# Optimization experiments

Measured on AMD Instinct MI355X. Metric: run time of the kernel, lower is better.

## Reference

```python
import jax, jax.numpy as jnp
import numpy as np

B, T, C, P = 512, 365, 10, 64  # batch, num_steps, input_dim, num_prototypes


def setup_inputs() -> dict:
    key = jax.random.key(0)
    k1, k2, k3, k4 = jax.random.split(key, 4)
    input_seq = jax.random.normal(k1, (B, T, C), dtype=jnp.float32)
    # binary observation mask (some dates missing)
    mask = (jax.random.uniform(k2, (B, T)) > 0.1).astype(jnp.float32)
    label = jax.random.randint(k3, (B,), 0, P)
    prototypes = jax.random.normal(k4, (P, T, C), dtype=jnp.float32)
    return {"input_seq": input_seq, "mask": mask, "label": label,
            "prototypes": prototypes}


def reference(input_seq, mask, label, prototypes):
    # distances[b,p] = sum_{t,c} mask[b,t] * (x[b,t,c] - proto[p,t,c])^2
    # expanded so we never materialize the [B,P,T,C] broadcast:
    #   = sum mask*x^2  - 2*sum mask*x*p + sum mask*p^2
    x2 = jnp.einsum('btc,btc,bt->b', input_seq, input_seq, mask)          # [B]
    xp = jnp.einsum('btc,bt,ptc->bp', input_seq, mask, prototypes)        # [B,P]
    p2 = jnp.einsum('bt,ptc,ptc->bp', mask, prototypes, prototypes)       # [B,P]
    distances = x2[:, None] - 2.0 * xp + p2                               # [B,P]
    indices = jnp.argmin(distances, axis=1)                               # [B]
    # gather selected prototype per sample (trans/offset inactive -> shared protos)
    output_seq = prototypes[indices]                                      # [B,T,C]
    return (output_seq, input_seq, distances, indices, label, mask)
```

## Files before the change

### kernel.cpp

```cpp
#include <hip/hip_runtime.h>

#define B_   512
#define T_   365
#define C_   10
#define P_   64
#define K_   3650
#define K2_  1825
#define KP_  3712
#define KP2_ 1856

#define OFF_OUT0 0u
#define OFF_IN   1868800u
#define OFF_DIST 3737600u
#define OFF_IDX  3770368u
#define OFF_LAB  3770880u
#define OFF_MASK 3771392u

__global__ __launch_bounds__(512, 4) void dist_kernel(
    const float* __restrict__ x, const float* __restrict__ mask,
    const float* __restrict__ protos, float* __restrict__ out)
{
    __shared__ float xm[2][KP_];
    __shared__ float mexp[2][KP_];
    __shared__ float mrow[2][368];

    const int tid  = threadIdx.x;
    const int lane = tid & 63;
    const int wv   = tid >> 6;
    const int bp   = blockIdx.x >> 1;
    const int ph   = blockIdx.x & 1;
    const int b0   = bp * 2;

    for (int t = tid; t < 2 * T_; t += 512) {
        int bb = t >= T_;
        int tt = t - bb * T_;
        float m = mask[(size_t)(b0 + bb) * T_ + tt];
        mrow[bb][tt] = m;
        if (ph == 0) out[OFF_MASK + (size_t)(b0 + bb) * T_ + tt] = m;
    }
    __syncthreads();

#pragma unroll
    for (int bb = 0; bb < 2; ++bb) {
        const float2* xr = (const float2*)(x + (size_t)(b0 + bb) * K_);
        float2*       er = (float2*)(out + OFF_IN + (size_t)(b0 + bb) * K_);
        float2*       sx = (float2*)&xm[bb][0];
        float2*       sm = (float2*)&mexp[bb][0];
        for (int i2 = tid; i2 < KP2_; i2 += 512) {
            float2 v = {0.f, 0.f}, mm = {0.f, 0.f};
            if (i2 < K2_) {
                v = xr[i2];
                if (ph == 0) er[i2] = v;
                int e = i2 * 2;
                mm.x = mrow[bb][e / C_];
                mm.y = mrow[bb][(e + 1) / C_];
                v.x *= mm.x;
                v.y *= mm.y;
            }
            sx[i2] = v;
            sm[i2] = mm;
        }
    }
    __syncthreads();

    const int p0 = ph * 32 + wv * 4;
    const float2* pr[4];
#pragma unroll
    for (int q = 0; q < 4; ++q)
        pr[q] = (const float2*)(protos + (size_t)(p0 + q) * K_);
    const float2* xr0 = (const float2*)&xm[0][0];
    const float2* xr1 = (const float2*)&xm[1][0];
    const float2* mr0 = (const float2*)&mexp[0][0];
    const float2* mr1 = (const float2*)&mexp[1][0];

    float acc0[4] = {0.f, 0.f, 0.f, 0.f};
    float acc1[4] = {0.f, 0.f, 0.f, 0.f};

#pragma unroll 4
    for (int it = 0; it < 29; ++it) {
        const int i2  = it * 64 + lane;
        const int i2c = i2 < K2_ ? i2 : (K2_ - 1);
        float2 pv[4];
#pragma unroll
        for (int q = 0; q < 4; ++q) pv[q] = pr[q][i2c];
        const float2 u0 = xr0[i2], m0 = mr0[i2];
        const float2 u1 = xr1[i2], m1 = mr1[i2];
#pragma unroll
        for (int q = 0; q < 4; ++q) {
            float tx, ty;
            tx = fmaf(-pv[q].x, m0.x, u0.x); acc0[q] = fmaf(tx, tx, acc0[q]);
            ty = fmaf(-pv[q].y, m0.y, u0.y); acc0[q] = fmaf(ty, ty, acc0[q]);
            tx = fmaf(-pv[q].x, m1.x, u1.x); acc1[q] = fmaf(tx, tx, acc1[q]);
            ty = fmaf(-pv[q].y, m1.y, u1.y); acc1[q] = fmaf(ty, ty, acc1[q]);
        }
    }

#pragma unroll
    for (int q = 0; q < 4; ++q) {
        float v0 = acc0[q], v1 = acc1[q];
        for (int off = 32; off; off >>= 1) {
            v0 += __shfl_down(v0, off);
            v1 += __shfl_down(v1, off);
        }
        if (lane == 0) {
            out[OFF_DIST + (size_t)b0 * P_ + p0 + q]       = v0;
            out[OFF_DIST + (size_t)(b0 + 1) * P_ + p0 + q] = v1;
        }
    }
}

__global__ __launch_bounds__(256) void argmin_kernel(
    const int* __restrict__ label, const float* __restrict__ protos,
    float* __restrict__ out)
{
    __shared__ int sel;
    const int b    = blockIdx.x;
    const int tid  = threadIdx.x;
    const int lane = tid & 63;

    if (tid < 64) {
        float v = out[OFF_DIST + (size_t)b * P_ + lane];
        int idx = lane;
        for (int off = 32; off; off >>= 1) {
            float ov = __shfl_down(v, off);
            int   oi = __shfl_down(idx, off);
            if (ov < v || (ov == v && oi < idx)) { v = ov; idx = oi; }
        }
        if (lane == 0) {
            sel = idx;
            out[OFF_IDX + b] = (float)idx;
            out[OFF_LAB + b] = (float)label[b];
        }
    }
    __syncthreads();

    const float2* src = (const float2*)(protos + (size_t)sel * K_);
    float2* dst = (float2*)(out + OFF_OUT0 + (size_t)b * K_);
    for (int i2 = tid; i2 < K2_; i2 += 256) dst[i2] = src[i2];
}

extern "C" void kernel_launch(void* const* d_in, const int* in_sizes, int n_in,
                              void* d_out, int out_size, void* d_ws, size_t ws_size,
                              hipStream_t stream) {
    const float* x      = (const float*)d_in[0];
    const float* mask   = (const float*)d_in[1];
    const int*   label  = (const int*)d_in[2];
    const float* protos = (const float*)d_in[3];
    float* out = (float*)d_out;

    dist_kernel<<<512, 512, 0, stream>>>(x, mask, protos, out);
    argmin_kernel<<<B_, 256, 0, stream>>>(label, protos, out);
}
```

Baseline: 90.37 us.

## Retile distance kernel to 8 samples x 16 prototypes using expanded-norm formulation

Each block now handles 8 batch rows and 16 prototypes instead of 2 rows and 32 prototypes, and each wave computes 2 prototypes for all 8 rows. The distance is computed as x2 - 2*xp + p2, with the mask folded in per time step, instead of as direct squared differences. x is read straight from global memory rather than staged through shared memory, so the large shared buffers are gone. The grid is halved to 256 blocks, which raises reuse of each prototype load but reduces parallelism and adds per-thread register pressure from 8-row accumulators. The expanded form can also shift floating-point rounding, which could change argmin ties.

```diff
diff --git a/kernel.cpp b/kernel.cpp
--- a/kernel.cpp
+++ b/kernel.cpp
@@ -1,13 +1,11 @@
 #include <hip/hip_runtime.h>
 
-#define B_   512
-#define T_   365
-#define C_   10
-#define P_   64
-#define K_   3650
-#define K2_  1825
-#define KP_  3712
-#define KP2_ 1856
+#define B_  512
+#define T_  365
+#define C_  10
+#define P_  64
+#define K_  3650
+#define K2_ 1825
 
 #define OFF_OUT0 0u
 #define OFF_IN   1868800u
@@ -20,91 +18,128 @@
     const float* __restrict__ x, const float* __restrict__ mask,
     const float* __restrict__ protos, float* __restrict__ out)
 {
-    __shared__ float xm[2][KP_];
-    __shared__ float mexp[2][KP_];
-    __shared__ float mrow[2][368];
+    __shared__ float mrow[8][372];
+    __shared__ float x2s[8];
 
     const int tid  = threadIdx.x;
     const int lane = tid & 63;
     const int wv   = tid >> 6;
-    const int bp   = blockIdx.x >> 1;
-    const int ph   = blockIdx.x & 1;
-    const int b0   = bp * 2;
+    const int g    = blockIdx.x >> 2;
+    const int q    = blockIdx.x & 3;
+    const int b0   = g * 8;
+    const int p0   = q * 16;
 
-    for (int t = tid; t < 2 * T_; t += 512) {
-        int bb = t >= T_;
-        int tt = t - bb * T_;
-        float m = mask[(size_t)(b0 + bb) * T_ + tt];
-        mrow[bb][tt] = m;
-        if (ph == 0) out[OFF_MASK + (size_t)(b0 + bb) * T_ + tt] = m;
+#pragma unroll
+    for (int r = 0; r < 8; ++r) {
+        if (tid < 372) {
+            float m = (tid < T_) ? mask[(size_t)(b0 + r) * T_ + tid] : 0.f;
+            mrow[r][tid] = m;
+            if (q == 0 && tid < T_)
+                out[OFF_MASK + (size_t)(b0 + r) * T_ + tid] = m;
+        }
+    }
+    __syncthreads();
+
+    const int pidx = p0 + wv * 2;
+    const float2* pr0 = (const float2*)(protos + (size_t)pidx * K_);
+    const float2* pr1 = (const float2*)(protos + (size_t)(pidx + 1) * K_);
+    const float2* xr[8];
+    float2*       er[8];
+#pragma unroll
+    for (int r = 0; r < 8; ++r) {
+        xr[r] = (const float2*)(x + (size_t)(b0 + r) * K_);
+        er[r] = (float2*)(out + OFF_IN + (size_t)(b0 + r) * K_);
+    }
+    const bool echo = (q == 0) && (wv == 0);
+    const bool dox2 = (wv == 0);
+
+    float2 a0[8], a1[8], xq[8];
+    float  c0[8], c1[8];
+#pragma unroll
+    for (int r = 0; r < 8; ++r) {
+        a0[r] = {0.f, 0.f}; a1[r] = {0.f, 0.f}; xq[r] = {0.f, 0.f};
+        c0[r] = 0.f; c1[r] = 0.f;
+    }
+
+    for (int it = 0; it < 28; ++it) {
+        const int i2 = it * 64 + lane;
+        const unsigned t = (unsigned)i2 / 5u;
+        const float2 pv0 = pr0[i2];
+        const float2 pv1 = pr1[i2];
+        const float s0 = fmaf(pv0.x, pv0.x, pv0.y * pv0.y);
+        const float s1 = fmaf(pv1.x, pv1.x, pv1.y * pv1.y);
+#pragma unroll
+        for (int r = 0; r < 8; ++r) {
+            const float  m  = mrow[r][t];
+            const float2 xv = xr[r][i2];
+            if (echo) er[r][i2] = xv;
+            float2 xmv;
+            xmv.x = xv.x * m;
+            xmv.y = xv.y * m;
+            a0[r].x = fmaf(xmv.x, pv0.x, a0[r].x);
+            a0[r].y = fmaf(xmv.y, pv0.y, a0[r].y);
+            a1[r].x = fmaf(xmv.x, pv1.x, a1[r].x);
+            a1[r].y = fmaf(xmv.y, pv1.y, a1[r].y);
+            c0[r] = fmaf(m, s0, c0[r]);
+            c1[r] = fmaf(m, s1, c1[r]);
+            if (dox2) {
+                xq[r].x = fmaf(xmv.x, xmv.x, xq[r].x);
+                xq[r].y = fmaf(xmv.y, xmv.y, xq[r].y);
+            }
+        }
+    }
+    {
+        const int i2 = 28 * 64 + lane;
+        if (i2 < K2_) {
+            const unsigned t = (unsigned)i2 / 5u;
+            const float2 pv0 = pr0[i2];
+            const float2 pv1 = pr1[i2];
+            const float s0 = fmaf(pv0.x, pv0.x, pv0.y * pv0.y);
+            const float s1 = fmaf(pv1.x, pv1.x, pv1.y * pv1.y);
+#pragma unroll
+            for (int r = 0; r < 8; ++r) {
+                const float  m  = mrow[r][t];
+                const float2 xv = xr[r][i2];
+                if (echo) er[r][i2] = xv;
+                float2 xmv;
+                xmv.x = xv.x * m;
+                xmv.y = xv.y * m;
+                a0[r].x = fmaf(xmv.x, pv0.x, a0[r].x);
+                a0[r].y = fmaf(xmv.y, pv0.y, a0[r].y);
+                a1[r].x = fmaf(xmv.x, pv1.x, a1[r].x);
+                a1[r].y = fmaf(xmv.y, pv1.y, a1[r].y);
+                c0[r] = fmaf(m, s0, c0[r]);
+                c1[r] = fmaf(m, s1, c1[r]);
+                if (dox2) {
+                    xq[r].x = fmaf(xmv.x, xmv.x, xq[r].x);
+                    xq[r].y = fmaf(xmv.y, xmv.y, xq[r].y);
+                }
+            }
+        }
+    }
+
+    if (dox2) {
+#pragma unroll
+        for (int r = 0; r < 8; ++r) {
+            float v = xq[r].x + xq[r].y;
+            for (int off = 32; off; off >>= 1) v += __shfl_down(v, off);
+            if (lane == 0) x2s[r] = v;
+        }
     }
     __syncthreads();
 
 #pragma unroll
-    for (int bb = 0; bb < 2; ++bb) {
-        const float2* xr = (const float2*)(x + (size_t)(b0 + bb) * K_);
-        float2*       er = (float2*)(out + OFF_IN + (size_t)(b0 + bb) * K_);
-        float2*       sx = (float2*)&xm[bb][0];
-        float2*       sm = (float2*)&mexp[bb][0];
-        for (int i2 = tid; i2 < KP2_; i2 += 512) {
-            float2 v = {0.f, 0.f}, mm = {0.f, 0.f};
-            if (i2 < K2_) {
-                v = xr[i2];
-                if (ph == 0) er[i2] = v;
-                int e = i2 * 2;
-                mm.x = mrow[bb][e / C_];
-                mm.y = mrow[bb][(e + 1) / C_];
-                v.x *= mm.x;
-                v.y *= mm.y;
-            }
-            sx[i2] = v;
-            sm[i2] = mm;
-        }
-    }
-    __syncthreads();
-
-    const int p0 = ph * 32 + wv * 4;
-    const float2* pr[4];
-#pragma unroll
-    for (int q = 0; q < 4; ++q)
-        pr[q] = (const float2*)(protos + (size_t)(p0 + q) * K_);
-    const float2* xr0 = (const float2*)&xm[0][0];
-    const float2* xr1 = (const float2*)&xm[1][0];
-    const float2* mr0 = (const float2*)&mexp[0][0];
-    const float2* mr1 = (const float2*)&mexp[1][0];
-
-    float acc0[4] = {0.f, 0.f, 0.f, 0.f};
-    float acc1[4] = {0.f, 0.f, 0.f, 0.f};
-
-#pragma unroll 4
-    for (int it = 0; it < 29; ++it) {
-        const int i2  = it * 64 + lane;
-        const int i2c = i2 < K2_ ? i2 : (K2_ - 1);
-        float2 pv[4];
-#pragma unroll
-        for (int q = 0; q < 4; ++q) pv[q] = pr[q][i2c];
-        const float2 u0 = xr0[i2], m0 = mr0[i2];
-        const float2 u1 = xr1[i2], m1 = mr1[i2];
-#pragma unroll
-        for (int q = 0; q < 4; ++q) {
-            float tx, ty;
-            tx = fmaf(-pv[q].x, m0.x, u0.x); acc0[q] = fmaf(tx, tx, acc0[q]);
-            ty = fmaf(-pv[q].y, m0.y, u0.y); acc0[q] = fmaf(ty, ty, acc0[q]);
-            tx = fmaf(-pv[q].x, m1.x, u1.x); acc1[q] = fmaf(tx, tx, acc1[q]);
-            ty = fmaf(-pv[q].y, m1.y, u1.y); acc1[q] = fmaf(ty, ty, acc1[q]);
-        }
-    }
-
-#pragma unroll
-    for (int q = 0; q < 4; ++q) {
-        float v0 = acc0[q], v1 = acc1[q];
+    for (int r = 0; r < 8; ++r) {
+        float v0 = fmaf(-2.f, a0[r].x + a0[r].y, c0[r]);
+        float v1 = fmaf(-2.f, a1[r].x + a1[r].y, c1[r]);
         for (int off = 32; off; off >>= 1) {
             v0 += __shfl_down(v0, off);
             v1 += __shfl_down(v1, off);
         }
         if (lane == 0) {
-            out[OFF_DIST + (size_t)b0 * P_ + p0 + q]       = v0;
-            out[OFF_DIST + (size_t)(b0 + 1) * P_ + p0 + q] = v1;
+            const float base = x2s[r];
+            out[OFF_DIST + (size_t)(b0 + r) * P_ + pidx]     = base + v0;
+            out[OFF_DIST + (size_t)(b0 + r) * P_ + pidx + 1] = base + v1;
         }
     }
 }
@@ -148,6 +183,6 @@
     const float* protos = (const float*)d_in[3];
     float* out = (float*)d_out;
 
-    dist_kernel<<<512, 512, 0, stream>>>(x, mask, protos, out);
+    dist_kernel<<<256, 512, 0, stream>>>(x, mask, protos, out);
     argmin_kernel<<<B_, 256, 0, stream>>>(label, protos, out);
 }
```

After: 145.5 us. +61.0%, slower.

## Use expanded distance form and block four batch rows per workgroup

Applied to the files above, without the earlier changes.

Replaces the direct masked squared-difference accumulation with the expanded form: a cross term x·m·p plus a mask-weighted p² term, with the x² term computed in the argmin kernel and added before the argmin. Each workgroup now handles four batch rows with 1024 threads and two prototypes per wave, which increases reuse of each prototype load. The per-element expanded mask buffer is dropped in favour of indexing the mask row by t. This cuts shared-memory traffic and FLOPs per prototype element, at the cost of possible floating-point cancellation differences and extra x/mask reads in the second kernel.

```diff
diff --git a/kernel.cpp b/kernel.cpp
--- a/kernel.cpp
+++ b/kernel.cpp
@@ -6,8 +6,8 @@
 #define P_   64
 #define K_   3650
 #define K2_  1825
-#define KP_  3712
 #define KP2_ 1856
+#define TP_  372
 
 #define OFF_OUT0 0u
 #define OFF_IN   1868800u
@@ -16,117 +16,140 @@
 #define OFF_LAB  3770880u
 #define OFF_MASK 3771392u
 
-__global__ __launch_bounds__(512, 4) void dist_kernel(
+__global__ __launch_bounds__(1024, 4) void dist_kernel(
     const float* __restrict__ x, const float* __restrict__ mask,
     const float* __restrict__ protos, float* __restrict__ out)
 {
-    __shared__ float xm[2][KP_];
-    __shared__ float mexp[2][KP_];
-    __shared__ float mrow[2][368];
+    __shared__ float xm[4][2 * KP2_];
+    __shared__ float mrow[4][TP_];
 
     const int tid  = threadIdx.x;
     const int lane = tid & 63;
     const int wv   = tid >> 6;
-    const int bp   = blockIdx.x >> 1;
-    const int ph   = blockIdx.x & 1;
-    const int b0   = bp * 2;
+    const int h    = blockIdx.x & 1;
+    const int g    = blockIdx.x >> 1;
+    const int b0   = g * 4;
 
-    for (int t = tid; t < 2 * T_; t += 512) {
-        int bb = t >= T_;
-        int tt = t - bb * T_;
-        float m = mask[(size_t)(b0 + bb) * T_ + tt];
-        mrow[bb][tt] = m;
-        if (ph == 0) out[OFF_MASK + (size_t)(b0 + bb) * T_ + tt] = m;
+    for (int j = tid; j < 4 * TP_; j += 1024) {
+        const int r = j / TP_;
+        const int t = j - r * TP_;
+        float m = 0.f;
+        if (t < T_) {
+            m = mask[(size_t)(b0 + r) * T_ + t];
+            if (h == 0) out[OFF_MASK + (size_t)(b0 + r) * T_ + t] = m;
+        }
+        mrow[r][t] = m;
     }
     __syncthreads();
 
 #pragma unroll
-    for (int bb = 0; bb < 2; ++bb) {
-        const float2* xr = (const float2*)(x + (size_t)(b0 + bb) * K_);
-        float2*       er = (float2*)(out + OFF_IN + (size_t)(b0 + bb) * K_);
-        float2*       sx = (float2*)&xm[bb][0];
-        float2*       sm = (float2*)&mexp[bb][0];
-        for (int i2 = tid; i2 < KP2_; i2 += 512) {
-            float2 v = {0.f, 0.f}, mm = {0.f, 0.f};
+    for (int r = 0; r < 4; ++r) {
+        const float2* xr = (const float2*)(x + (size_t)(b0 + r) * K_);
+        float2*       er = (float2*)(out + OFF_IN + (size_t)(b0 + r) * K_);
+        float2*       sx = (float2*)&xm[r][0];
+        for (int i2 = tid; i2 < KP2_; i2 += 1024) {
+            float2 v = {0.f, 0.f};
             if (i2 < K2_) {
                 v = xr[i2];
-                if (ph == 0) er[i2] = v;
-                int e = i2 * 2;
-                mm.x = mrow[bb][e / C_];
-                mm.y = mrow[bb][(e + 1) / C_];
-                v.x *= mm.x;
-                v.y *= mm.y;
+                if (h == 0) er[i2] = v;
+                const unsigned t = (unsigned)i2 / 5u;
+                const float m = mrow[r][t];
+                v.x *= m;
+                v.y *= m;
             }
             sx[i2] = v;
-            sm[i2] = mm;
         }
     }
     __syncthreads();
 
-    const int p0 = ph * 32 + wv * 4;
-    const float2* pr[4];
+    const int pidx = h * 32 + wv * 2;
+    const float2* pr0 = (const float2*)(protos + (size_t)pidx * K_);
+    const float2* pr1 = (const float2*)(protos + (size_t)(pidx + 1) * K_);
+
+    float2 a0[4], a1[4];
+    float  c0[4], c1[4];
 #pragma unroll
-    for (int q = 0; q < 4; ++q)
-        pr[q] = (const float2*)(protos + (size_t)(p0 + q) * K_);
-    const float2* xr0 = (const float2*)&xm[0][0];
-    const float2* xr1 = (const float2*)&xm[1][0];
-    const float2* mr0 = (const float2*)&mexp[0][0];
-    const float2* mr1 = (const float2*)&mexp[1][0];
-
-    float acc0[4] = {0.f, 0.f, 0.f, 0.f};
-    float acc1[4] = {0.f, 0.f, 0.f, 0.f};
+    for (int r = 0; r < 4; ++r) {
+        a0[r] = {0.f, 0.f}; a1[r] = {0.f, 0.f};
+        c0[r] = 0.f; c1[r] = 0.f;
+    }
 
 #pragma unroll 4
     for (int it = 0; it < 29; ++it) {
         const int i2  = it * 64 + lane;
         const int i2c = i2 < K2_ ? i2 : (K2_ - 1);
-        float2 pv[4];
+        const unsigned t = (unsigned)i2 / 5u;
+        const float2 pv0 = pr0[i2c];
+        const float2 pv1 = pr1[i2c];
+        const float s0 = fmaf(pv0.x, pv0.x, pv0.y * pv0.y);
+        const float s1 = fmaf(pv1.x, pv1.x, pv1.y * pv1.y);
 #pragma unroll
-        for (int q = 0; q < 4; ++q) pv[q] = pr[q][i2c];
-        const float2 u0 = xr0[i2], m0 = mr0[i2];
-        const float2 u1 = xr1[i2], m1 = mr1[i2];
-#pragma unroll
-        for (int q = 0; q < 4; ++q) {
-            float tx, ty;
-            tx = fmaf(-pv[q].x, m0.x, u0.x); acc0[q] = fmaf(tx, tx, acc0[q]);
-            ty = fmaf(-pv[q].y, m0.y, u0.y); acc0[q] = fmaf(ty, ty, acc0[q]);
-            tx = fmaf(-pv[q].x, m1.x, u1.x); acc1[q] = fmaf(tx, tx, acc1[q]);
-            ty = fmaf(-pv[q].y, m1.y, u1.y); acc1[q] = fmaf(ty, ty, acc1[q]);
+        for (int r = 0; r < 4; ++r) {
+            const float2 u = ((const float2*)&xm[r][0])[i2];
+            const float  m = mrow[r][t];
+            a0[r].x = fmaf(u.x, pv0.x, a0[r].x);
+            a0[r].y = fmaf(u.y, pv0.y, a0[r].y);
+            a1[r].x = fmaf(u.x, pv1.x, a1[r].x);
+            a1[r].y = fmaf(u.y, pv1.y, a1[r].y);
+            c0[r] = fmaf(m, s0, c0[r]);
+            c1[r] = fmaf(m, s1, c1[r]);
         }
     }
 
 #pragma unroll
-    for (int q = 0; q < 4; ++q) {
-        float v0 = acc0[q], v1 = acc1[q];
+    for (int r = 0; r < 4; ++r) {
+        float v0 = fmaf(-2.f, a0[r].x + a0[r].y, c0[r]);
+        float v1 = fmaf(-2.f, a1[r].x + a1[r].y, c1[r]);
         for (int off = 32; off; off >>= 1) {
             v0 += __shfl_down(v0, off);
             v1 += __shfl_down(v1, off);
         }
         if (lane == 0) {
-            out[OFF_DIST + (size_t)b0 * P_ + p0 + q]       = v0;
-            out[OFF_DIST + (size_t)(b0 + 1) * P_ + p0 + q] = v1;
+            out[OFF_DIST + (size_t)(b0 + r) * P_ + pidx]     = v0;
+            out[OFF_DIST + (size_t)(b0 + r) * P_ + pidx + 1] = v1;
         }
     }
 }
 
 __global__ __launch_bounds__(256) void argmin_kernel(
+    const float* __restrict__ x, const float* __restrict__ mask,
     const int* __restrict__ label, const float* __restrict__ protos,
     float* __restrict__ out)
 {
-    __shared__ int sel;
+    __shared__ float red[4];
+    __shared__ float x2sh;
+    __shared__ int   sel;
+
     const int b    = blockIdx.x;
     const int tid  = threadIdx.x;
     const int lane = tid & 63;
+    const int wv   = tid >> 6;
+
+    const float2* xr = (const float2*)(x + (size_t)b * K_);
+    const float*  mr = mask + (size_t)b * T_;
+    float s = 0.f;
+    for (int i2 = tid; i2 < K2_; i2 += 256) {
+        const float2 v = xr[i2];
+        const float  m = mr[(unsigned)i2 / 5u];
+        s = fmaf(m, fmaf(v.x, v.x, v.y * v.y), s);
+    }
+    for (int off = 32; off; off >>= 1) s += __shfl_down(s, off);
+    if (lane == 0) red[wv] = s;
+    __syncthreads();
+    if (tid == 0) x2sh = red[0] + red[1] + red[2] + red[3];
+    __syncthreads();
 
     if (tid < 64) {
-        float v = out[OFF_DIST + (size_t)b * P_ + lane];
-        int idx = lane;
+        const float x2 = x2sh;
+        float v = out[OFF_DIST + (size_t)b * P_ + tid] + x2;
+        out[OFF_DIST + (size_t)b * P_ + tid] = v;
+        int idx = tid;
         for (int off = 32; off; off >>= 1) {
             float ov = __shfl_down(v, off);
             int   oi = __shfl_down(idx, off);
             if (ov < v || (ov == v && oi < idx)) { v = ov; idx = oi; }
         }
-        if (lane == 0) {
+        if (tid == 0) {
             sel = idx;
             out[OFF_IDX + b] = (float)idx;
             out[OFF_LAB + b] = (float)label[b];
@@ -148,6 +171,6 @@
     const float* protos = (const float*)d_in[3];
     float* out = (float*)d_out;
 
-    dist_kernel<<<512, 512, 0, stream>>>(x, mask, protos, out);
-    argmin_kernel<<<B_, 256, 0, stream>>>(label, protos, out);
+    dist_kernel<<<256, 1024, 0, stream>>>(x, mask, protos, out);
+    argmin_kernel<<<B_, 256, 0, stream>>>(x, mask, label, protos, out);
 }
```

After: 91.73 us. No clear change (+1.5%).
